# Optimization experiments

Hardware: AMD Instinct MI355X
Metric: run time of the kernel (lower is better)

The kernel has to match this reference:

```python
import jax, jax.numpy as jnp
import numpy as np
import math

EPS = 1e-6


def setup_inputs() -> dict:
    key = jax.random.key(0)
    k1, k2, k3 = jax.random.split(key, 3)
    B, S, D = 8, 2048, 256
    return {
        "query": jax.random.normal(k1, (B, S, D), dtype=jnp.float32),
        "keys": jax.random.normal(k2, (B, S, D), dtype=jnp.float32),
        "values": jax.random.normal(k3, (B, S, D), dtype=jnp.float32),
        "c": jnp.asarray(0.01, dtype=jnp.float32),  # learned curvature parameter
    }


def reference(query, keys, values, c):
    # query/keys: [B,S,D], values: [B,S,Dv]
    scale = math.sqrt(query.shape[-1])
    q2 = jnp.sum(query * query, axis=-1)            # [B,S]  |q_i|^2
    k2 = jnp.sum(keys * keys, axis=-1)              # [B,S]  |k_j|^2
    cross = jnp.einsum("bid,bjd->bij", query, keys)  # [B,S,S]
    # squared pairwise distance via identity, avoiding the [B,S,S,D] diff tensor
    nd2 = jnp.maximum(q2[:, :, None] + k2[:, None, :] - 2.0 * cross, 0.0)
    # faithful to original: denom pairs query row i with key row i (broadcast quirk)
    denom = jnp.maximum((1.0 - c * q2) * (1.0 - c * k2), EPS)  # [B,S]
    arg = jnp.maximum(1.0 + 2.0 * c * nd2 / denom[:, :, None], 1.0 + EPS)
    dist = jnp.arccosh(arg)                          # [B,S,S]
    attn = jax.nn.softmax(-dist / scale, axis=-1)
    return jnp.einsum("bij,bjd->bid", attn, values)
```

## Files before the change

### kernel.cpp

```cpp
#include <hip/hip_runtime.h>

#define B_N   8
#define S_LEN 2048
#define D_DIM 256
#define Q4    512
#define JT    32
#define NIT   16

typedef __attribute__((ext_vector_type(4)))  float          f32x4;
typedef __attribute__((ext_vector_type(16))) float          f32x16;
typedef __attribute__((ext_vector_type(8)))  short          s16x8;
typedef __attribute__((ext_vector_type(8)))  __bf16         b16x8;
typedef __attribute__((ext_vector_type(8)))  unsigned short u16x8;
typedef __attribute__((ext_vector_type(4)))  unsigned int   u32x4;

__device__ __forceinline__ unsigned short f2bf(float f) {
    unsigned u = __builtin_bit_cast(unsigned, f);
    u += 0x7FFFu + ((u >> 16) & 1u);
    return (unsigned short)(u >> 16);
}
__device__ __forceinline__ u16x8 pack8(f32x4 a, f32x4 b) {
    u16x8 o;
#pragma unroll
    for (int u = 0; u < 4; ++u) { o[u] = f2bf(a[u]); o[u + 4] = f2bf(b[u]); }
    return o;
}
__device__ __forceinline__ f32x16 zero16() {
    f32x16 z;
#pragma unroll
    for (int i = 0; i < 16; ++i) z[i] = 0.f;
    return z;
}
__device__ __forceinline__ unsigned cvtpk(float lo, float hi) {
    unsigned r;
    asm("v_cvt_pk_bf16_f32 %0, %1, %2" : "=v"(r) : "v"(lo), "v"(hi));
    return r;
}
__device__ __forceinline__ void xswap(unsigned& x, unsigned& y, int lh) {
    unsigned vs = lh ? x : y;
    unsigned vr = (unsigned)__shfl_xor((int)vs, 32, 64);
    x = lh ? vr : x;
    y = lh ? y : vr;
}
__device__ __forceinline__ float hw_sqrt(float x) {
    float r; asm("v_sqrt_f32 %0, %1" : "=v"(r) : "v"(x)); return r;
}
__device__ __forceinline__ float hw_log2(float x) {
    float r; asm("v_log_f32 %0, %1" : "=v"(r) : "v"(x)); return r;
}
__device__ __forceinline__ float hw_exp2(float x) {
    float r; asm("v_exp_f32 %0, %1" : "=v"(r) : "v"(x)); return r;
}
__device__ __forceinline__ void gload16(const void* g, void* l) {
    __builtin_amdgcn_global_load_lds((const __attribute__((address_space(1))) void*)g,
                                     (__attribute__((address_space(3))) void*)l, 16, 0, 0);
}

template <typename A>
__device__ __forceinline__ auto mfma3216_(A a, A b, f32x16 c, int)
    -> decltype(__builtin_amdgcn_mfma_f32_32x32x16_bf16(a, b, c, 0, 0, 0)) {
    return __builtin_amdgcn_mfma_f32_32x32x16_bf16(a, b, c, 0, 0, 0);
}
template <typename A>
__device__ __forceinline__ f32x16 mfma3216_(A a, A b, f32x16 c, long) {
    b16x8 a2 = __builtin_bit_cast(b16x8, a);
    b16x8 b2 = __builtin_bit_cast(b16x8, b);
    return __builtin_amdgcn_mfma_f32_32x32x16_bf16(a2, b2, c, 0, 0, 0);
}
__device__ __forceinline__ f32x16 MFMA(u16x8 a, u16x8 b, f32x16 c) {
    return mfma3216_(__builtin_bit_cast(s16x8, a), __builtin_bit_cast(s16x8, b), c, 0);
}

__global__ void __launch_bounds__(256) prep_rows(const float* __restrict__ Q,
                                                 const float* __restrict__ K,
                                                 const float* __restrict__ cp,
                                                 float* __restrict__ q2g,
                                                 float* __restrict__ k2g,
                                                 float* __restrict__ cfg) {
    const int w = threadIdx.x >> 6, l = threadIdx.x & 63;
    const float c = *cp;
#pragma unroll 1
    for (int p = 0; p < 16; ++p) {
        const int row = blockIdx.x * 64 + p * 4 + w;
        f32x4 qv = *((const f32x4*)(Q + (size_t)row * D_DIM) + l);
        f32x4 kv = *((const f32x4*)(K + (size_t)row * D_DIM) + l);
        float sq = qv[0]*qv[0] + qv[1]*qv[1] + qv[2]*qv[2] + qv[3]*qv[3];
        float sk = kv[0]*kv[0] + kv[1]*kv[1] + kv[2]*kv[2] + kv[3]*kv[3];
#pragma unroll
        for (int m = 1; m < 64; m <<= 1) {
            sq += __shfl_xor(sq, m, 64);
            sk += __shfl_xor(sk, m, 64);
        }
        if (l == 0) {
            q2g[row] = sq;
            k2g[row] = sk;
            float dn = fmaxf((1.f - c * sq) * (1.f - c * sk), 1e-6f);
            cfg[row] = 2.f * c / dn;
        }
    }
}

__global__ void __launch_bounds__(256) cvt_bf16(const float* __restrict__ src,
                                                unsigned short* __restrict__ dst) {
    const size_t i = ((size_t)blockIdx.x * 256 + threadIdx.x) * 8;
    f32x4 a = *(const f32x4*)(src + i);
    f32x4 b = *(const f32x4*)(src + i + 4);
    *(u16x8*)(dst + i) = pack8(a, b);
}

__global__ void __launch_bounds__(256) transp_v(const float* __restrict__ V,
                                                unsigned short* __restrict__ VT) {
    __shared__ float tile[64][65];
    const int bid = blockIdx.x;
    const int b = bid >> 7, rem = bid & 127, jt = rem >> 2, dt = rem & 3;
    const int j0 = jt * 64, d0 = dt * 64;
    const int t = threadIdx.x;
#pragma unroll
    for (int p = 0; p < 4; ++p) {
        const int jr = p * 16 + (t >> 4);
        f32x4 v = *(const f32x4*)(V + (size_t)(b * S_LEN + j0 + jr) * D_DIM + d0 + (t & 15) * 4);
#pragma unroll
        for (int u = 0; u < 4; ++u) tile[jr][(t & 15) * 4 + u] = v[u];
    }
    __syncthreads();
#pragma unroll
    for (int p = 0; p < 2; ++p) {
        const int dr = p * 32 + (t >> 3), seg = t & 7;
        u16x8 o;
#pragma unroll
        for (int u = 0; u < 8; ++u) o[u] = f2bf(tile[seg * 8 + u][dr]);
        *(u16x8*)(VT + (size_t)(b * D_DIM + d0 + dr) * S_LEN + j0 + seg * 8) = o;
    }
}

template <int PRE>
__global__ void __launch_bounds__(512, 2) hyp_attn(
    const float* __restrict__ Qf, const float* __restrict__ Kf, const float* __restrict__ Vf,
    const unsigned short* __restrict__ Kb, const unsigned short* __restrict__ VTg,
    const float* __restrict__ q2g, const float* __restrict__ k2g, const float* __restrict__ cfg,
    float* __restrict__ out) {
    __shared__ __align__(1024) unsigned char tiles[131072];
    __shared__ float k2sh[S_LEN];
    __shared__ float lsumBuf[4][2][32];

    const int bid = blockIdx.x;
    const int nb = (bid & 7) * 32 + (bid >> 3);
    const int b = nb >> 5, rt = nb & 31;
    const int tid = threadIdx.x;
    const int w = tid >> 6, l = tid & 63;
    const int l31 = l & 31, lh = l >> 5;
    const int qg = w & 1, qt = w >> 1;
    const int qr0 = rt * 64 + qg * 32;
    const int qrow = b * S_LEN + qr0 + l31;

    *(f32x4*)&k2sh[tid * 4] = *(const f32x4*)(k2g + b * S_LEN + tid * 4);

    u16x8 qf[16];
    {
        const float* qp = Qf + (size_t)qrow * D_DIM + lh * 8;
#pragma unroll
        for (int ks = 0; ks < 16; ++ks) {
            f32x4 a = *(const f32x4*)(qp + ks * 16);
            f32x4 c4 = *(const f32x4*)(qp + ks * 16 + 4);
            qf[ks] = pack8(a, c4);
        }
    }
    const float q2r = q2g[qrow];
    const float cfr = cfg[qrow];
    const float base1 = fmaf(cfr, q2r, 1.0f);

    f32x16 oacc[8];
#pragma unroll
    for (int i = 0; i < 8; ++i) oacc[i] = zero16();
    float lsum = 0.f;

    const size_t kbBase = (size_t)b * S_LEN * D_DIM;
    const int xk = (l31 & 7) << 4;
    const int xv = (l31 & 3) << 4;
    const char* kq = (const char*)tiles + qt * 16384 + l31 * 512;
    const char* vq = (const char*)tiles + 65536 + qt * 16384 + l31 * 64;

#pragma unroll 1
    for (int it = 0; it < NIT; ++it) {
        __syncthreads();
        const int jb0 = it * JT;
        if (PRE) {
#pragma unroll
            for (int p = 0; p < 8; ++p) {
                const int cc = p * 512 + tid;
                const int qc = cc >> 10, rr = (cc >> 5) & 31, seg = cc & 31;
                const unsigned short* gp = Kb + kbBase + (size_t)(qc * Q4 + jb0 + rr) * D_DIM
                                         + ((seg ^ (rr & 7)) << 3);
                gload16(gp, (char*)tiles + cc * 16);
            }
#pragma unroll
            for (int p = 0; p < 8; ++p) {
                const int cc = p * 512 + tid;
                const int qc = cc >> 10, dr = (cc >> 2) & 255, sl = cc & 3;
                const unsigned short* gp = VTg + ((size_t)b * D_DIM + dr) * S_LEN
                                         + qc * Q4 + jb0 + ((sl ^ (dr & 3)) << 3);
                gload16(gp, (char*)tiles + 65536 + cc * 16);
            }
        } else {
#pragma unroll
            for (int p = 0; p < 8; ++p) {
                const int cc = p * 512 + tid;
                const int qc = cc >> 10, rr = (cc >> 5) & 31, seg = cc & 31;
                const float* sp = Kf + kbBase + (size_t)(qc * Q4 + jb0 + rr) * D_DIM
                                + ((seg ^ (rr & 7)) << 3);
                *(u16x8*)((char*)tiles + cc * 16) = pack8(*(const f32x4*)sp, *(const f32x4*)(sp + 4));
            }
#pragma unroll
            for (int p = 0; p < 8; ++p) {
                const int cc = p * 512 + tid;
                const int qc = cc >> 10, jj = (cc >> 5) & 31, dg = cc & 31;
                const float* sp = Vf + kbBase + (size_t)(qc * Q4 + jb0 + jj) * D_DIM + dg * 8;
                f32x4 a = *(const f32x4*)sp, c4 = *(const f32x4*)(sp + 4);
#pragma unroll
                for (int u = 0; u < 8; ++u) {
                    const int d = dg * 8 + u;
                    const float x = u < 4 ? a[u] : c4[u - 4];
                    *(unsigned short*)((char*)tiles + 65536 + qc * 16384 + d * 64
                                       + ((jj * 2) ^ ((d & 3) << 4))) = f2bf(x);
                }
            }
        }
        __syncthreads();

        f32x16 sacc = zero16();
#pragma unroll
        for (int ks = 0; ks < 16; ++ks) {
            u16x8 kf = *(const u16x8*)(kq + ((((ks * 2 + lh) << 4) ^ xk)));
            sacc = MFMA(kf, qf[ks], sacc);
        }

        float pvv[16];
#pragma unroll
        for (int r = 0; r < 16; ++r) {
            const int crow = (r & 3) + 8 * (r >> 2) + 4 * lh;
            const float k2j = k2sh[qt * Q4 + jb0 + crow];
            const float t = fmaf(-2.f, sacc[r], k2j);
            const float arg = fmaxf(fmaf(cfr, t, base1), 1.f + 1e-6f);
            const float y = arg + hw_sqrt(fmaf(arg, arg, -1.f));
            const float p = hw_exp2(hw_log2(y) * -0.0625f);
            lsum += p;
            pvv[r] = p;
        }

        unsigned A_ = cvtpk(pvv[0], pvv[1]),   C_ = cvtpk(pvv[2], pvv[3]);
        unsigned Bv = cvtpk(pvv[4], pvv[5]),   D_ = cvtpk(pvv[6], pvv[7]);
        unsigned E_ = cvtpk(pvv[8], pvv[9]),   G_ = cvtpk(pvv[10], pvv[11]);
        unsigned F_ = cvtpk(pvv[12], pvv[13]), H_ = cvtpk(pvv[14], pvv[15]);
        xswap(A_, Bv, lh); xswap(C_, D_, lh);
        xswap(E_, F_, lh); xswap(G_, H_, lh);
        const u16x8 pa0 = __builtin_bit_cast(u16x8, (u32x4){A_, C_, Bv, D_});
        const u16x8 pa1 = __builtin_bit_cast(u16x8, (u32x4){E_, G_, F_, H_});

#pragma unroll
        for (int db = 0; db < 8; ++db) {
            u16x8 vf0 = *(const u16x8*)(vq + db * 2048 + ((lh << 4) ^ xv));
            oacc[db] = MFMA(pa0, vf0, oacc[db]);
            u16x8 vf1 = *(const u16x8*)(vq + db * 2048 + (((2 + lh) << 4) ^ xv));
            oacc[db] = MFMA(pa1, vf1, oacc[db]);
        }
    }

    lsum += __shfl_xor(lsum, 32, 64);
    __syncthreads();
    if (lh == 0) lsumBuf[qt][qg][l31] = lsum;
    float* sf = (float*)tiles;
    if (qt >= 2) {
        const int slot = (qt - 2) * 2 + qg;
#pragma unroll
        for (int db = 0; db < 8; ++db)
#pragma unroll
            for (int r = 0; r < 16; ++r) {
                const int crow = (r & 3) + 8 * (r >> 2) + 4 * lh;
                sf[slot * 8192 + crow * 256 + db * 32 + l31] = oacc[db][r];
            }
    }
    __syncthreads();
    if (qt <= 1) {
        const int slot = qt * 2 + qg;
#pragma unroll
        for (int db = 0; db < 8; ++db)
#pragma unroll
            for (int r = 0; r < 16; ++r) {
                const int crow = (r & 3) + 8 * (r >> 2) + 4 * lh;
                oacc[db][r] += sf[slot * 8192 + crow * 256 + db * 32 + l31];
            }
    }
    __syncthreads();
    if (qt == 1) {
#pragma unroll
        for (int db = 0; db < 8; ++db)
#pragma unroll
            for (int r = 0; r < 16; ++r) {
                const int crow = (r & 3) + 8 * (r >> 2) + 4 * lh;
                sf[qg * 8192 + crow * 256 + db * 32 + l31] = oacc[db][r];
            }
    }
    __syncthreads();
    if (qt == 0) {
        float rdn[16];
#pragma unroll
        for (int r = 0; r < 16; ++r) {
            const int crow = (r & 3) + 8 * (r >> 2) + 4 * lh;
            rdn[r] = 1.0f / (lsumBuf[0][qg][crow] + lsumBuf[1][qg][crow] +
                             lsumBuf[2][qg][crow] + lsumBuf[3][qg][crow]);
        }
#pragma unroll
        for (int db = 0; db < 8; ++db)
#pragma unroll
            for (int r = 0; r < 16; ++r) {
                const int crow = (r & 3) + 8 * (r >> 2) + 4 * lh;
                const float o = oacc[db][r] + sf[qg * 8192 + crow * 256 + db * 32 + l31];
                out[(size_t)(b * S_LEN + qr0 + crow) * D_DIM + db * 32 + l31] = o * rdn[r];
            }
    }
}

extern "C" void kernel_launch(void* const* d_in, const int* in_sizes, int n_in,
                              void* d_out, int out_size, void* d_ws, size_t ws_size,
                              hipStream_t stream) {
    const float* Q = (const float*)d_in[0];
    const float* K = (const float*)d_in[1];
    const float* V = (const float*)d_in[2];
    const float* cp = (const float*)d_in[3];
    float* out = (float*)d_out;
    (void)in_sizes; (void)n_in; (void)out_size;

    const size_t BS = (size_t)B_N * S_LEN;
    float* q2g = (float*)d_ws;
    float* k2g = q2g + BS;
    float* cfg = k2g + BS;
    unsigned short* Kb = (unsigned short*)(cfg + BS);
    unsigned short* VTg = Kb + BS * D_DIM;
    const size_t need_full = 3 * BS * 4 + 2 * BS * D_DIM * 2;

    prep_rows<<<(B_N * S_LEN) / 64, 256, 0, stream>>>(Q, K, cp, q2g, k2g, cfg);

    if (ws_size >= need_full) {
        cvt_bf16<<<(int)((BS * D_DIM / 8) / 256), 256, 0, stream>>>(K, Kb);
        transp_v<<<B_N * (S_LEN / 64) * (D_DIM / 64), 256, 0, stream>>>(V, VTg);
        hyp_attn<1><<<256, 512, 0, stream>>>(Q, K, V, Kb, VTg, q2g, k2g, cfg, out);
    } else {
        hyp_attn<0><<<256, 512, 0, stream>>>(Q, K, V, Kb, VTg, q2g, k2g, cfg, out);
    }
}
```

Measured before the change: 129.5 us.

## Restructure attention block to 4 waves with 2-way key split and smaller LDS tile

```diff
diff --git a/kernel.cpp b/kernel.cpp
--- a/kernel.cpp
+++ b/kernel.cpp
@@ -3,9 +3,6 @@
 #define B_N   8
 #define S_LEN 2048
 #define D_DIM 256
-#define Q4    512
-#define JT    32
-#define NIT   16
 
 typedef __attribute__((ext_vector_type(4)))  float          f32x4;
 typedef __attribute__((ext_vector_type(16))) float          f32x16;
@@ -50,6 +47,9 @@
 }
 __device__ __forceinline__ float hw_exp2(float x) {
     float r; asm("v_exp_f32 %0, %1" : "=v"(r) : "v"(x)); return r;
+}
+__device__ __forceinline__ float hw_rcp(float x) {
+    float r; asm("v_rcp_f32 %0, %1" : "=v"(r) : "v"(x)); return r;
 }
 __device__ __forceinline__ void gload16(const void* g, void* l) {
     __builtin_amdgcn_global_load_lds((const __attribute__((address_space(1))) void*)g,
@@ -134,14 +134,14 @@
 }
 
 template <int PRE>
-__global__ void __launch_bounds__(512, 2) hyp_attn(
+__global__ void __launch_bounds__(256, 2) hyp_attn(
     const float* __restrict__ Qf, const float* __restrict__ Kf, const float* __restrict__ Vf,
     const unsigned short* __restrict__ Kb, const unsigned short* __restrict__ VTg,
     const float* __restrict__ q2g, const float* __restrict__ k2g, const float* __restrict__ cfg,
     float* __restrict__ out) {
-    __shared__ __align__(1024) unsigned char tiles[131072];
+    __shared__ __align__(1024) unsigned char tiles[65536];
     __shared__ float k2sh[S_LEN];
-    __shared__ float lsumBuf[4][2][32];
+    __shared__ float lsumBuf[2][2][32];
 
     const int bid = blockIdx.x;
     const int nb = (bid & 7) * 32 + (bid >> 3);
@@ -149,11 +149,12 @@
     const int tid = threadIdx.x;
     const int w = tid >> 6, l = tid & 63;
     const int l31 = l & 31, lh = l >> 5;
-    const int qg = w & 1, qt = w >> 1;
+    const int qg = w >> 1, jsub = w & 1;
     const int qr0 = rt * 64 + qg * 32;
     const int qrow = b * S_LEN + qr0 + l31;
 
-    *(f32x4*)&k2sh[tid * 4] = *(const f32x4*)(k2g + b * S_LEN + tid * 4);
+    *(f32x4*)&k2sh[tid * 8]     = *(const f32x4*)(k2g + b * S_LEN + tid * 8);
+    *(f32x4*)&k2sh[tid * 8 + 4] = *(const f32x4*)(k2g + b * S_LEN + tid * 8 + 4);
 
     u16x8 qf[16];
     {
@@ -175,82 +176,85 @@
     float lsum = 0.f;
 
     const size_t kbBase = (size_t)b * S_LEN * D_DIM;
+
+    auto stage = [&](int it) {
+        const int j0 = it * 64;
+        if (PRE) {
+#pragma unroll
+            for (int p = 0; p < 8; ++p) {
+                const int idx = p * 256 + tid;
+                const int row = idx >> 5, sl = idx & 31;
+                const unsigned short* gp = Kb + kbBase + (size_t)(j0 + row) * D_DIM
+                                         + ((sl ^ (row & 7)) << 3);
+                gload16(gp, (char*)tiles + idx * 16);
+            }
+#pragma unroll
+            for (int p = 0; p < 8; ++p) {
+                const int idx = p * 256 + tid;
+                const int d = idx >> 3, sl = idx & 7;
+                const unsigned short* gp = VTg + ((size_t)b * D_DIM + d) * S_LEN + j0
+                                         + ((sl ^ (d & 7)) << 3);
+                gload16(gp, (char*)tiles + 32768 + idx * 16);
+            }
+        } else {
+#pragma unroll
+            for (int p = 0; p < 8; ++p) {
+                const int idx = p * 256 + tid;
+                const int row = idx >> 5, sl = idx & 31;
+                const float* sp = Kf + kbBase + (size_t)(j0 + row) * D_DIM
+                                + ((sl ^ (row & 7)) << 3);
+                *(u16x8*)((char*)tiles + idx * 16) =
+                    pack8(*(const f32x4*)sp, *(const f32x4*)(sp + 4));
+            }
+#pragma unroll
+            for (int p = 0; p < 8; ++p) {
+                const int idx = p * 256 + tid;
+                const int d = idx >> 3, sl = idx & 7;
+                const int jj = (sl ^ (d & 7)) << 3;
+                u16x8 o;
+#pragma unroll
+                for (int u = 0; u < 8; ++u)
+                    o[u] = f2bf(Vf[kbBase + (size_t)(j0 + jj + u) * D_DIM + d]);
+                *(u16x8*)((char*)tiles + 32768 + idx * 16) = o;
+            }
+        }
+    };
+
     const int xk = (l31 & 7) << 4;
-    const int xv = (l31 & 3) << 4;
-    const char* kq = (const char*)tiles + qt * 16384 + l31 * 512;
-    const char* vq = (const char*)tiles + 65536 + qt * 16384 + l31 * 64;
+    const char* KBp = (const char*)tiles + (jsub * 32 + l31) * 512;
+    const char* VBp = (const char*)tiles + 32768 + l31 * 128;
 
 #pragma unroll 1
-    for (int it = 0; it < NIT; ++it) {
+    for (int it = 0; it < 32; ++it) {
+        stage(it);
         __syncthreads();
-        const int jb0 = it * JT;
-        if (PRE) {
-#pragma unroll
-            for (int p = 0; p < 8; ++p) {
-                const int cc = p * 512 + tid;
-                const int qc = cc >> 10, rr = (cc >> 5) & 31, seg = cc & 31;
-                const unsigned short* gp = Kb + kbBase + (size_t)(qc * Q4 + jb0 + rr) * D_DIM
-                                         + ((seg ^ (rr & 7)) << 3);
-                gload16(gp, (char*)tiles + cc * 16);
-            }
-#pragma unroll
-            for (int p = 0; p < 8; ++p) {
-                const int cc = p * 512 + tid;
-                const int qc = cc >> 10, dr = (cc >> 2) & 255, sl = cc & 3;
-                const unsigned short* gp = VTg + ((size_t)b * D_DIM + dr) * S_LEN
-                                         + qc * Q4 + jb0 + ((sl ^ (dr & 3)) << 3);
-                gload16(gp, (char*)tiles + 65536 + cc * 16);
-            }
-        } else {
-#pragma unroll
-            for (int p = 0; p < 8; ++p) {
-                const int cc = p * 512 + tid;
-                const int qc = cc >> 10, rr = (cc >> 5) & 31, seg = cc & 31;
-                const float* sp = Kf + kbBase + (size_t)(qc * Q4 + jb0 + rr) * D_DIM
-                                + ((seg ^ (rr & 7)) << 3);
-                *(u16x8*)((char*)tiles + cc * 16) = pack8(*(const f32x4*)sp, *(const f32x4*)(sp + 4));
-            }
-#pragma unroll
-            for (int p = 0; p < 8; ++p) {
-                const int cc = p * 512 + tid;
-                const int qc = cc >> 10, jj = (cc >> 5) & 31, dg = cc & 31;
-                const float* sp = Vf + kbBase + (size_t)(qc * Q4 + jb0 + jj) * D_DIM + dg * 8;
-                f32x4 a = *(const f32x4*)sp, c4 = *(const f32x4*)(sp + 4);
-#pragma unroll
-                for (int u = 0; u < 8; ++u) {
-                    const int d = dg * 8 + u;
-                    const float x = u < 4 ? a[u] : c4[u - 4];
-                    *(unsigned short*)((char*)tiles + 65536 + qc * 16384 + d * 64
-                                       + ((jj * 2) ^ ((d & 3) << 4))) = f2bf(x);
-                }
-            }
-        }
-        __syncthreads();
 
         f32x16 sacc = zero16();
 #pragma unroll
         for (int ks = 0; ks < 16; ++ks) {
-            u16x8 kf = *(const u16x8*)(kq + ((((ks * 2 + lh) << 4) ^ xk)));
+            u16x8 kf = *(const u16x8*)(KBp + (((ks * 2 + lh) << 4) ^ xk));
             sacc = MFMA(kf, qf[ks], sacc);
         }
 
-        float pvv[16];
+        f32x4 k2q[4];
+#pragma unroll
+        for (int g = 0; g < 4; ++g)
+            k2q[g] = *(const f32x4*)&k2sh[it * 64 + jsub * 32 + g * 8 + lh * 4];
+
 #pragma unroll
         for (int r = 0; r < 16; ++r) {
-            const int crow = (r & 3) + 8 * (r >> 2) + 4 * lh;
-            const float k2j = k2sh[qt * Q4 + jb0 + crow];
-            const float t = fmaf(-2.f, sacc[r], k2j);
+            const float t = fmaf(-2.f, sacc[r], k2q[r >> 2][r & 3]);
             const float arg = fmaxf(fmaf(cfr, t, base1), 1.f + 1e-6f);
             const float y = arg + hw_sqrt(fmaf(arg, arg, -1.f));
             const float p = hw_exp2(hw_log2(y) * -0.0625f);
             lsum += p;
-            pvv[r] = p;
-        }
-
-        unsigned A_ = cvtpk(pvv[0], pvv[1]),   C_ = cvtpk(pvv[2], pvv[3]);
-        unsigned Bv = cvtpk(pvv[4], pvv[5]),   D_ = cvtpk(pvv[6], pvv[7]);
-        unsigned E_ = cvtpk(pvv[8], pvv[9]),   G_ = cvtpk(pvv[10], pvv[11]);
-        unsigned F_ = cvtpk(pvv[12], pvv[13]), H_ = cvtpk(pvv[14], pvv[15]);
+            sacc[r] = p;
+        }
+
+        unsigned A_ = cvtpk(sacc[0], sacc[1]),   C_ = cvtpk(sacc[2], sacc[3]);
+        unsigned Bv = cvtpk(sacc[4], sacc[5]),   D_ = cvtpk(sacc[6], sacc[7]);
+        unsigned E_ = cvtpk(sacc[8], sacc[9]),   G_ = cvtpk(sacc[10], sacc[11]);
+        unsigned F_ = cvtpk(sacc[12], sacc[13]), H_ = cvtpk(sacc[14], sacc[15]);
         xswap(A_, Bv, lh); xswap(C_, D_, lh);
         xswap(E_, F_, lh); xswap(G_, H_, lh);
         const u16x8 pa0 = __builtin_bit_cast(u16x8, (u32x4){A_, C_, Bv, D_});
@@ -258,40 +262,20 @@
 
 #pragma unroll
         for (int db = 0; db < 8; ++db) {
-            u16x8 vf0 = *(const u16x8*)(vq + db * 2048 + ((lh << 4) ^ xv));
+            u16x8 vf0 = *(const u16x8*)(VBp + db * 4096 +
+                                        (((jsub * 4 + lh) << 4) ^ xk));
             oacc[db] = MFMA(pa0, vf0, oacc[db]);
-            u16x8 vf1 = *(const u16x8*)(vq + db * 2048 + (((2 + lh) << 4) ^ xv));
+            u16x8 vf1 = *(const u16x8*)(VBp + db * 4096 +
+                                        (((jsub * 4 + 2 + lh) << 4) ^ xk));
             oacc[db] = MFMA(pa1, vf1, oacc[db]);
         }
+        __syncthreads();
     }
 
     lsum += __shfl_xor(lsum, 32, 64);
-    __syncthreads();
-    if (lh == 0) lsumBuf[qt][qg][l31] = lsum;
+    if (lh == 0) lsumBuf[jsub][qg][l31] = lsum;
     float* sf = (float*)tiles;
-    if (qt >= 2) {
-        const int slot = (qt - 2) * 2 + qg;
-#pragma unroll
-        for (int db = 0; db < 8; ++db)
-#pragma unroll
-            for (int r = 0; r < 16; ++r) {
-                const int crow = (r & 3) + 8 * (r >> 2) + 4 * lh;
-                sf[slot * 8192 + crow * 256 + db * 32 + l31] = oacc[db][r];
-            }
-    }
-    __syncthreads();
-    if (qt <= 1) {
-        const int slot = qt * 2 + qg;
-#pragma unroll
-        for (int db = 0; db < 8; ++db)
-#pragma unroll
-            for (int r = 0; r < 16; ++r) {
-                const int crow = (r & 3) + 8 * (r >> 2) + 4 * lh;
-                oacc[db][r] += sf[slot * 8192 + crow * 256 + db * 32 + l31];
-            }
-    }
-    __syncthreads();
-    if (qt == 1) {
+    if (jsub == 1) {
 #pragma unroll
         for (int db = 0; db < 8; ++db)
 #pragma unroll
@@ -301,13 +285,12 @@
             }
     }
     __syncthreads();
-    if (qt == 0) {
+    if (jsub == 0) {
         float rdn[16];
 #pragma unroll
         for (int r = 0; r < 16; ++r) {
             const int crow = (r & 3) + 8 * (r >> 2) + 4 * lh;
-            rdn[r] = 1.0f / (lsumBuf[0][qg][crow] + lsumBuf[1][qg][crow] +
-                             lsumBuf[2][qg][crow] + lsumBuf[3][qg][crow]);
+            rdn[r] = hw_rcp(lsumBuf[0][qg][crow] + lsumBuf[1][qg][crow]);
         }
 #pragma unroll
         for (int db = 0; db < 8; ++db)
@@ -343,8 +326,8 @@
     if (ws_size >= need_full) {
         cvt_bf16<<<(int)((BS * D_DIM / 8) / 256), 256, 0, stream>>>(K, Kb);
         transp_v<<<B_N * (S_LEN / 64) * (D_DIM / 64), 256, 0, stream>>>(V, VTg);
-        hyp_attn<1><<<256, 512, 0, stream>>>(Q, K, V, Kb, VTg, q2g, k2g, cfg, out);
+        hyp_attn<1><<<256, 256, 0, stream>>>(Q, K, V, Kb, VTg, q2g, k2g, cfg, out);
     } else {
-        hyp_attn<0><<<256, 512, 0, stream>>>(Q, K, V, Kb, VTg, q2g, k2g, cfg, out);
-    }
-}
+        hyp_attn<0><<<256, 256, 0, stream>>>(Q, K, V, Kb, VTg, q2g, k2g, cfg, out);
+    }
+}
```

Result: slower. 163.4 us (+26.2%).
